# Kernel tuning notes

Measured on AMD Instinct MI355X. Metric: run time of the kernel, lower is better.

Reference implementation:

```python
import jax, jax.numpy as jnp
import numpy as np

ALPHA = 1.0
DIAG_FILL = 500000.0


def _batch_pairwise_dist(x, y):
    # x: [B, Nx, D], y: [B, Ny, D] -> squared-distance matrix [B, Nx, Ny]
    xx = jnp.sum(x * x, axis=-1)  # [B, Nx]
    yy = jnp.sum(y * y, axis=-1)  # [B, Ny]
    zz = jnp.einsum('bnd,bmd->bnm', x, y)  # [B, Nx, Ny]
    return xx[:, :, None] + yy[:, None, :] - 2.0 * zz


def setup_inputs() -> dict:
    key = jax.random.key(0)
    k1, k2 = jax.random.split(key)
    B, N, D = 4, 4096, 3
    gts = jax.random.normal(k1, (B, N, D), dtype=jnp.float32)
    preds = jax.random.normal(k2, (B, N, D), dtype=jnp.float32)
    return {"gts": gts, "preds": preds}


def reference(gts, preds):
    # Cross-term Chamfer: P[b,i,j] = ||gts_i - preds_j||^2
    P = _batch_pairwise_dist(gts, preds)  # [B, Ng, Np]
    loss_1 = jnp.sum(jnp.min(P, axis=1), axis=1)  # min over gts, sum over preds
    loss_2 = jnp.sum(jnp.min(P, axis=2), axis=1)  # min over preds, sum over gts

    # Self nearest-neighbor distance distributions (diagonal masked out)
    Ng = gts.shape[1]
    Np = preds.shape[1]
    eye_g = jnp.eye(Ng, dtype=bool)
    eye_p = jnp.eye(Np, dtype=bool)
    P1 = jnp.where(eye_g[None, :, :], DIAG_FILL, _batch_pairwise_dist(gts, gts))
    P2 = jnp.where(eye_p[None, :, :], DIAG_FILL, _batch_pairwise_dist(preds, preds))

    mins1 = jnp.sort(jnp.min(P1, axis=1), axis=1)  # [B, Ng]
    mins2 = jnp.sort(jnp.min(P2, axis=1), axis=1)  # [B, Np]
    min_ps = min(mins1.shape[1], mins2.shape[1])
    loss_ordering = jnp.sum((mins1[:, :min_ps] - mins2[:, :min_ps]) ** 2, axis=1)

    return loss_1 + loss_2 + ALPHA * loss_ordering
```

## Files before the change

### kernel.cpp

```cpp
#include <hip/hip_runtime.h>

constexpr int BATCH = 4;
constexpr int NPTS  = 4096;
constexpr int QC    = 1024;
constexpr int TC    = 512;
constexpr int NTHR  = 256;
constexpr int QPT   = QC / NTHR;


__global__ __launch_bounds__(256) void nn_init(unsigned int* __restrict__ m) {
    int i = blockIdx.x * blockDim.x + threadIdx.x;
    m[i] = 0x7F800000u;
}

__global__ __launch_bounds__(NTHR) void nn_pass(const float* __restrict__ gts,
                                                const float* __restrict__ preds,
                                                unsigned int* __restrict__ nnmin) {
    const int pass  = blockIdx.z & 3;
    const int b     = blockIdx.z >> 2;
    const int qbase = blockIdx.y * QC;
    const int tbase = blockIdx.x * TC;
    const bool selfp = (pass >= 2);
    const float* __restrict__ A = (pass == 0 || pass == 2) ? gts : preds;
    const float* __restrict__ T = (pass == 1 || pass == 2) ? gts : preds;

    __shared__ float4 tp[TC];
    for (int k = threadIdx.x; k < TC; k += NTHR) {
        const float* p = T + ((size_t)b * NPTS + tbase + k) * 3;
        tp[k] = make_float4(p[0], p[1], p[2], 0.f);
    }
    __syncthreads();

    float qx[QPT], qy[QPT], qz[QPT], mn[QPT];
    int qidx[QPT];
#pragma unroll
    for (int q = 0; q < QPT; ++q) {
        const int qi = qbase + threadIdx.x + q * NTHR;
        qidx[q] = qi;
        const float* p = A + ((size_t)b * NPTS + qi) * 3;
        qx[q] = p[0]; qy[q] = p[1]; qz[q] = p[2];
        mn[q] = 1e30f;
    }

    if (selfp) {
#pragma unroll 4
        for (int j = 0; j < TC; ++j) {
            const float4 t = tp[j];
            const int tj = tbase + j;
#pragma unroll
            for (int q = 0; q < QPT; ++q) {
                const float dx = qx[q] - t.x, dy = qy[q] - t.y, dz = qz[q] - t.z;
                float d = dx * dx;
                d = fmaf(dy, dy, d);
                d = fmaf(dz, dz, d);
                d = (tj == qidx[q]) ? 1e30f : d;
                mn[q] = fminf(mn[q], d);
            }
        }
    } else {
#pragma unroll 4
        for (int j = 0; j < TC; ++j) {
            const float4 t = tp[j];
#pragma unroll
            for (int q = 0; q < QPT; ++q) {
                const float dx = qx[q] - t.x, dy = qy[q] - t.y, dz = qz[q] - t.z;
                float d = dx * dx;
                d = fmaf(dy, dy, d);
                d = fmaf(dz, dz, d);
                mn[q] = fminf(mn[q], d);
            }
        }
    }

    unsigned int* dst = nnmin + ((size_t)pass * BATCH + b) * NPTS;
#pragma unroll
    for (int q = 0; q < QPT; ++q)
        atomicMin(&dst[qidx[q]], __float_as_uint(mn[q]));
}

__global__ __launch_bounds__(1024) void nn_sort(unsigned int* __restrict__ nnmin) {
    const int which = blockIdx.x & 1;
    const int b     = blockIdx.x >> 1;
    unsigned int* src = nnmin + ((size_t)(2 + which) * BATCH + b) * NPTS;
    __shared__ float s[NPTS];
    for (int i = threadIdx.x; i < NPTS; i += 1024) s[i] = __uint_as_float(src[i]);

    for (int k = 2; k <= NPTS; k <<= 1) {
        for (int j = k >> 1; j > 0; j >>= 1) {
            __syncthreads();
#pragma unroll
            for (int t = threadIdx.x; t < NPTS / 2; t += 1024) {
                const int i = ((t & ~(j - 1)) << 1) | (t & (j - 1));
                const int p = i | j;
                const bool up = ((i & k) == 0);
                const float a = s[i], c = s[p];
                if ((a > c) == up) { s[i] = c; s[p] = a; }
            }
        }
    }
    __syncthreads();
    for (int i = threadIdx.x; i < NPTS; i += 1024) src[i] = __float_as_uint(s[i]);
}

__global__ __launch_bounds__(512) void nn_reduce(const unsigned int* __restrict__ nnmin,
                                                 float* __restrict__ out) {
    const int b = blockIdx.x;
    const int tid = threadIdx.x;
    __shared__ float red[512];

    const unsigned int* m0 = nnmin + ((size_t)0 * BATCH + b) * NPTS;
    const unsigned int* m1 = nnmin + ((size_t)1 * BATCH + b) * NPTS;
    const unsigned int* s1 = nnmin + ((size_t)2 * BATCH + b) * NPTS;
    const unsigned int* s2 = nnmin + ((size_t)3 * BATCH + b) * NPTS;

    float acc = 0.f;
    for (int i = tid; i < NPTS; i += 512) {
        acc += __uint_as_float(m0[i]) + __uint_as_float(m1[i]);
        const float d = __uint_as_float(s1[i]) - __uint_as_float(s2[i]);
        acc = fmaf(d, d, acc);
    }

    red[tid] = acc;
    __syncthreads();
    for (int s = 256; s > 0; s >>= 1) {
        if (tid < s) red[tid] += red[tid + s];
        __syncthreads();
    }
    if (tid == 0) out[b] = red[0];
}

extern "C" void kernel_launch(void* const* d_in, const int* in_sizes, int n_in,
                              void* d_out, int out_size, void* d_ws, size_t ws_size,
                              hipStream_t stream) {
    const float* gts   = (const float*)d_in[0];
    const float* preds = (const float*)d_in[1];
    float* out = (float*)d_out;
    unsigned int* nnmin = (unsigned int*)d_ws;

    nn_init<<<(4 * BATCH * NPTS) / 256, 256, 0, stream>>>(nnmin);
    dim3 grid(NPTS / TC, NPTS / QC, BATCH * 4);
    nn_pass<<<grid, NTHR, 0, stream>>>(gts, preds, nnmin);
    nn_sort<<<2 * BATCH, 1024, 0, stream>>>(nnmin);
    nn_reduce<<<BATCH, 512, 0, stream>>>(nnmin, out);
}
```

Before: 132.9 us.

## Fuse sort and reduce into one kernel with register-resident wave bitonic sort

Replaces the shared-memory bitonic sort kernel and the separate reduce kernel with a single kernel per batch. Two waves each sort 4096 values held in registers (64 per lane), using lane shuffles for cross-lane stages and in-register compare-swaps otherwise. Meanwhile two other waves sum the cross-term minima with vectorised loads. The init kernel is replaced by a memset to 0x7F bytes, which gives a large positive float that still works as the atomicMin sentinel. This removes a kernel launch and the barrier-heavy shared-memory sort, at the cost of high register pressure (64-float arrays) and only one sorting wave per array.

```diff
diff --git a/kernel.cpp b/kernel.cpp
--- a/kernel.cpp
+++ b/kernel.cpp
@@ -7,11 +7,6 @@
 constexpr int NTHR  = 256;
 constexpr int QPT   = QC / NTHR;
 
-
-__global__ __launch_bounds__(256) void nn_init(unsigned int* __restrict__ m) {
-    int i = blockIdx.x * blockDim.x + threadIdx.x;
-    m[i] = 0x7F800000u;
-}
 
 __global__ __launch_bounds__(NTHR) void nn_pass(const float* __restrict__ gts,
                                                 const float* __restrict__ preds,
@@ -78,51 +73,97 @@
         atomicMin(&dst[qidx[q]], __float_as_uint(mn[q]));
 }
 
-__global__ __launch_bounds__(1024) void nn_sort(unsigned int* __restrict__ nnmin) {
-    const int which = blockIdx.x & 1;
-    const int b     = blockIdx.x >> 1;
-    unsigned int* src = nnmin + ((size_t)(2 + which) * BATCH + b) * NPTS;
-    __shared__ float s[NPTS];
-    for (int i = threadIdx.x; i < NPTS; i += 1024) s[i] = __uint_as_float(src[i]);
+__global__ __launch_bounds__(256) void nn_final(const unsigned int* __restrict__ nnmin,
+                                                float* __restrict__ out) {
+    const int b    = blockIdx.x;
+    const int tid  = threadIdx.x;
+    const int wave = tid >> 6;
+    const int lane = tid & 63;
+    __shared__ float sA[NPTS];
+    __shared__ float sB[NPTS];
+    __shared__ float red[256];
 
-    for (int k = 2; k <= NPTS; k <<= 1) {
-        for (int j = k >> 1; j > 0; j >>= 1) {
-            __syncthreads();
+    float part = 0.f;
+
+    if (wave < 2) {
+        const unsigned int* src = nnmin + ((size_t)(2 + wave) * BATCH + b) * NPTS;
+        float v[64];
 #pragma unroll
-            for (int t = threadIdx.x; t < NPTS / 2; t += 1024) {
-                const int i = ((t & ~(j - 1)) << 1) | (t & (j - 1));
-                const int p = i | j;
-                const bool up = ((i & k) == 0);
-                const float a = s[i], c = s[p];
-                if ((a > c) == up) { s[i] = c; s[p] = a; }
+        for (int e4 = 0; e4 < 16; ++e4) {
+            const uint4 u = reinterpret_cast<const uint4*>(src)[lane * 16 + e4];
+            v[e4 * 4 + 0] = __uint_as_float(u.x);
+            v[e4 * 4 + 1] = __uint_as_float(u.y);
+            v[e4 * 4 + 2] = __uint_as_float(u.z);
+            v[e4 * 4 + 3] = __uint_as_float(u.w);
+        }
+
+#pragma unroll
+        for (int lk = 1; lk <= 12; ++lk) {
+            const int k = 1 << lk;
+#pragma unroll
+            for (int lj = lk - 1; lj >= 0; --lj) {
+                const int j = 1 << lj;
+                if (j >= 64) {
+                    const int lm = j >> 6;
+                    const bool asc = ((lane & (k >> 6)) == 0);
+                    const bool keepmin = (((lane & lm) == 0) == asc);
+#pragma unroll
+                    for (int e = 0; e < 64; ++e) {
+                        const float pv = __shfl_xor(v[e], lm, 64);
+                        v[e] = keepmin ? fminf(v[e], pv) : fmaxf(v[e], pv);
+                    }
+                } else if (k >= 64) {
+                    const bool asc = ((lane & (k >> 6)) == 0);
+#pragma unroll
+                    for (int e = 0; e < 64; ++e) {
+                        if ((e & j) == 0) {
+                            const int p = e | j;
+                            const float a = v[e], c = v[p];
+                            v[e] = asc ? fminf(a, c) : fmaxf(a, c);
+                            v[p] = asc ? fmaxf(a, c) : fminf(a, c);
+                        }
+                    }
+                } else {
+#pragma unroll
+                    for (int e = 0; e < 64; ++e) {
+                        if ((e & j) == 0) {
+                            const int p = e | j;
+                            const bool asc = ((e & k) == 0);
+                            const float a = v[e], c = v[p];
+                            v[e] = asc ? fminf(a, c) : fmaxf(a, c);
+                            v[p] = asc ? fmaxf(a, c) : fminf(a, c);
+                        }
+                    }
+                }
             }
+        }
+
+        float* dst = (wave == 0) ? sA : sB;
+#pragma unroll
+        for (int e = 0; e < 64; ++e) dst[e * 64 + lane] = v[e];
+    } else {
+        const int local = tid - 128;
+        const float* m0 = (const float*)(nnmin + ((size_t)0 * BATCH + b) * NPTS);
+        const float* m1 = (const float*)(nnmin + ((size_t)1 * BATCH + b) * NPTS);
+#pragma unroll
+        for (int i = 0; i < 8; ++i) {
+            const float4 u0 = reinterpret_cast<const float4*>(m0)[local + 128 * i];
+            const float4 u1 = reinterpret_cast<const float4*>(m1)[local + 128 * i];
+            part += u0.x + u0.y + u0.z + u0.w + u1.x + u1.y + u1.z + u1.w;
         }
     }
     __syncthreads();
-    for (int i = threadIdx.x; i < NPTS; i += 1024) src[i] = __float_as_uint(s[i]);
-}
 
-__global__ __launch_bounds__(512) void nn_reduce(const unsigned int* __restrict__ nnmin,
-                                                 float* __restrict__ out) {
-    const int b = blockIdx.x;
-    const int tid = threadIdx.x;
-    __shared__ float red[512];
-
-    const unsigned int* m0 = nnmin + ((size_t)0 * BATCH + b) * NPTS;
-    const unsigned int* m1 = nnmin + ((size_t)1 * BATCH + b) * NPTS;
-    const unsigned int* s1 = nnmin + ((size_t)2 * BATCH + b) * NPTS;
-    const unsigned int* s2 = nnmin + ((size_t)3 * BATCH + b) * NPTS;
-
-    float acc = 0.f;
-    for (int i = tid; i < NPTS; i += 512) {
-        acc += __uint_as_float(m0[i]) + __uint_as_float(m1[i]);
-        const float d = __uint_as_float(s1[i]) - __uint_as_float(s2[i]);
-        acc = fmaf(d, d, acc);
+#pragma unroll
+    for (int e = 0; e < 16; ++e) {
+        const int t = tid + 256 * e;
+        const float d = sA[t] - sB[t];
+        part = fmaf(d, d, part);
     }
 
-    red[tid] = acc;
+    red[tid] = part;
     __syncthreads();
-    for (int s = 256; s > 0; s >>= 1) {
+    for (int s = 128; s > 0; s >>= 1) {
         if (tid < s) red[tid] += red[tid + s];
         __syncthreads();
     }
@@ -137,9 +178,8 @@
     float* out = (float*)d_out;
     unsigned int* nnmin = (unsigned int*)d_ws;
 
-    nn_init<<<(4 * BATCH * NPTS) / 256, 256, 0, stream>>>(nnmin);
+    hipMemsetAsync(d_ws, 0x7F, (size_t)4 * BATCH * NPTS * sizeof(unsigned int), stream);
     dim3 grid(NPTS / TC, NPTS / QC, BATCH * 4);
     nn_pass<<<grid, NTHR, 0, stream>>>(gts, preds, nnmin);
-    nn_sort<<<2 * BATCH, 1024, 0, stream>>>(nnmin);
-    nn_reduce<<<BATCH, 512, 0, stream>>>(nnmin, out);
+    nn_final<<<BATCH, 256, 0, stream>>>(nnmin, out);
 }
```

Measured after the change: 412.8 us. +210.7%, slower.
